# Kernel tuning notes

Hardware: AMD Instinct MI355X
Metric: run time of the kernel (lower is better)

Reference implementation:

```python
import jax, jax.numpy as jnp
import numpy as np
import math

B, S, D, H = 2, 2048, 2048, 16
HD = D // H  # head_dim = 128


def _rope_tables(seq_len, head_dim, theta=10000.0):
    inv = 1.0 / (theta ** (np.arange(0, head_dim, 2, dtype=np.float32) / head_dim))
    t = np.arange(seq_len, dtype=np.float32)
    freqs = np.outer(t, inv)  # [S, HD/2]
    return jnp.asarray(np.cos(freqs)), jnp.asarray(np.sin(freqs))


def setup_inputs() -> dict:
    key = jax.random.key(0)
    ks = jax.random.split(key, 6)
    std = 1.0 / math.sqrt(D)
    x = jax.random.normal(ks[0], (B, S, D), dtype=jnp.float32)
    wq_w = jax.random.normal(ks[1], (D, D), dtype=jnp.float32) * std
    wk_w = jax.random.normal(ks[2], (D, D), dtype=jnp.float32) * std
    wv_w = jax.random.normal(ks[3], (D, D), dtype=jnp.float32) * std
    wo_w = jax.random.normal(ks[4], (D, D), dtype=jnp.float32) * std
    zb = jnp.zeros((D,), dtype=jnp.float32)
    fc, fs = _rope_tables(S, HD)
    return {"x": x, "wq_w": wq_w, "wq_b": zb, "wk_w": wk_w, "wk_b": zb,
            "wv_w": wv_w, "wv_b": zb, "wo_w": wo_w, "wo_b": zb,
            "freqs_cos": fc, "freqs_sin": fs}


def _apply_rope(q, k, cos, sin):
    # q, k: [B, S, H, HD]; cos/sin: [S, HD/2] -> broadcast [1, S, 1, HD/2]
    cos = cos[None, :, None, :]
    sin = sin[None, :, None, :]

    def rot(t):
        tr, ti = t[..., 0::2], t[..., 1::2]
        orr = tr * cos - ti * sin
        oi = tr * sin + ti * cos
        return jnp.stack([orr, oi], axis=-1).reshape(t.shape)

    return rot(q), rot(k)


def reference(x, wq_w, wq_b, wk_w, wk_b, wv_w, wv_b, wo_w, wo_b, freqs_cos, freqs_sin):
    b, s, d = x.shape
    q = (x @ wq_w.T + wq_b).reshape(b, s, H, HD)
    k = (x @ wk_w.T + wk_b).reshape(b, s, H, HD)
    v = (x @ wv_w.T + wv_b).reshape(b, s, H, HD)
    q, k = _apply_rope(q, k, freqs_cos[:s], freqs_sin[:s])
    q = q.transpose(0, 2, 1, 3)  # [B,H,S,HD]
    k = k.transpose(0, 2, 1, 3)
    v = v.transpose(0, 2, 1, 3)
    scale = math.sqrt(HD)
    scores = jnp.einsum('bhqd,bhkd->bhqk', q, k) / scale
    causal = jnp.tril(jnp.ones((s, s), dtype=bool))
    scores = jnp.where(causal[None, None], scores, jnp.float32(-jnp.inf))
    attn = jax.nn.softmax(scores, axis=-1)
    out = jnp.einsum('bhqk,bhkd->bhqd', attn, v)
    out = out.transpose(0, 2, 1, 3).reshape(b, s, d)
    out = out @ wo_w.T + wo_b
    return out, k, v
```

## Files before the change

kernel.cpp:

```cpp
#include <hip/hip_runtime.h>

#define B_  2
#define S_  2048
#define D_  2048
#define H_  16
#define HD_ 128

#define QSCALE 0.1275174319003887f

typedef __attribute__((ext_vector_type(4))) float  f32x4;
typedef __attribute__((ext_vector_type(8))) short  short8;
typedef __attribute__((ext_vector_type(8))) __bf16 bf16x8;
typedef __attribute__((ext_vector_type(4))) float  floatv4;
typedef __attribute__((ext_vector_type(4))) unsigned short ushortv4;

__device__ inline unsigned short f2bf(float f) {
  unsigned int u = __builtin_bit_cast(unsigned int, f);
  u += 0x7fffu + ((u >> 16) & 1u);
  return (unsigned short)(u >> 16);
}

__device__ inline void gld16(void* lds, const void* g) {
  __builtin_amdgcn_global_load_lds(
      (const __attribute__((address_space(1))) unsigned int*)g,
      (__attribute__((address_space(3))) unsigned int*)lds, 16, 0, 0);
}

__device__ inline bf16x8 lds_frag(const unsigned short* p) {
  return __builtin_bit_cast(bf16x8, *(const short8*)p);
}
__device__ inline bf16x8 lds_frag_b(const void* p) {
  return __builtin_bit_cast(bf16x8, *(const short8*)p);
}

__global__ void cvt_all(const float* __restrict__ x,
                        const float* __restrict__ w0, const float* __restrict__ w1,
                        const float* __restrict__ w2, const float* __restrict__ w3,
                        unsigned short* __restrict__ xb,
                        unsigned short* __restrict__ wb0, unsigned short* __restrict__ wb1,
                        unsigned short* __restrict__ wb2, unsigned short* __restrict__ wb3) {
  int i = blockIdx.x * 256 + threadIdx.x;
  const float* s; unsigned short* d; int off;
  if (i < 2097152) { s = x; d = xb; off = i; }
  else {
    int j = i - 2097152;
    int r = j >> 20; off = j & 1048575;
    s = (r == 0) ? w0 : (r == 1) ? w1 : (r == 2) ? w2 : w3;
    d = (r == 0) ? wb0 : (r == 1) ? wb1 : (r == 2) ? wb2 : wb3;
  }
  floatv4 v = ((const floatv4*)s)[off];
  ushortv4 o;
  o.x = f2bf(v.x); o.y = f2bf(v.y); o.z = f2bf(v.z); o.w = f2bf(v.w);
  ((ushortv4*)d)[off] = o;
}

__global__ __launch_bounds__(256, 2)
void gemm_nt(const unsigned short* __restrict__ A,
             const unsigned short* __restrict__ W,
             const float* __restrict__ bias,
             float* __restrict__ C, int M, int N, int K) {
  __shared__ __attribute__((aligned(16))) unsigned short As[128 * 32];
  __shared__ __attribute__((aligned(16))) unsigned short Bs[128 * 32];
  const int t = threadIdx.x;
  const int w = t >> 6, lane = t & 63;
  const int quad = lane >> 4, l16 = lane & 15;
  const int m0 = blockIdx.y * 128, n0 = blockIdx.x * 128;
  const int wm = (w >> 1) * 64, wn = (w & 1) * 64;
  f32x4 acc[4][4] = {};

  for (int k0 = 0; k0 < K; k0 += 32) {
    __syncthreads();
#pragma unroll
    for (int j = 0; j < 2; ++j) {
      int o = (t + 256 * j) * 16;
      int row = o >> 6, cb = o & 63;
      gld16((char*)As + w * 1024 + j * 4096,
            (const char*)(A + (size_t)(m0 + row) * K + k0) + cb);
      gld16((char*)Bs + w * 1024 + j * 4096,
            (const char*)(W + (size_t)(n0 + row) * K + k0) + cb);
    }
    __syncthreads();
    bf16x8 af[4], bfr[4];
#pragma unroll
    for (int i = 0; i < 4; ++i)
      af[i] = lds_frag(As + (wm + i * 16 + l16) * 32 + quad * 8);
#pragma unroll
    for (int j = 0; j < 4; ++j)
      bfr[j] = lds_frag(Bs + (wn + j * 16 + l16) * 32 + quad * 8);
#pragma unroll
    for (int i = 0; i < 4; ++i)
#pragma unroll
      for (int j = 0; j < 4; ++j)
        acc[i][j] = __builtin_amdgcn_mfma_f32_16x16x32_bf16(af[i], bfr[j], acc[i][j], 0, 0, 0);
  }

#pragma unroll
  for (int j = 0; j < 4; ++j) {
    int col = n0 + wn + j * 16 + l16;
    float bv = bias[col];
#pragma unroll
    for (int i = 0; i < 4; ++i)
#pragma unroll
      for (int r = 0; r < 4; ++r) {
        int row = m0 + wm + i * 16 + quad * 4 + r;
        C[(size_t)row * N + col] = acc[i][j][r] + bv;
      }
  }
}

template<int MI0, int NJ0>
__device__ inline void quad_mm(f32x4 (&acc)[4][4], const bf16x8 (&af)[2][2], const bf16x8 (&bf)[2][2]) {
#pragma unroll
  for (int mi = 0; mi < 2; ++mi)
#pragma unroll
    for (int nj = 0; nj < 2; ++nj)
#pragma unroll
      for (int ks = 0; ks < 2; ++ks)
        acc[MI0 + mi][NJ0 + nj] =
            __builtin_amdgcn_mfma_f32_16x16x32_bf16(af[mi][ks], bf[nj][ks], acc[MI0 + mi][NJ0 + nj], 0, 0, 0);
}

__device__ inline void stage(char* ldsbuf, int chunk, const char* gtile, int w, long thrOff) {
  gld16(ldsbuf + chunk * 8192 + w * 1024, gtile + (long)chunk * 64 * 4096 + thrOff);
}

#define RDF(dst, buf, baserow)                                                          \
  do {                                                                                  \
    int _r0 = (baserow);                                                                \
    _Pragma("unroll") for (int _ii = 0; _ii < 2; ++_ii) {                               \
      int _row = _r0 + _ii * 16;                                                        \
      _Pragma("unroll") for (int _ks = 0; _ks < 2; ++_ks)                               \
          dst[_ii][_ks] = lds_frag_b((buf) + _row * 128 + ((_ks * 64 + quad * 16) ^ xsw)); \
    }                                                                                   \
  } while (0)

#define GBAR() __builtin_amdgcn_s_barrier()
#define LGK0()                                                 \
  do {                                                         \
    asm volatile("s_waitcnt lgkmcnt(0)" ::: "memory");         \
    __builtin_amdgcn_sched_barrier(0);                         \
  } while (0)

template<bool QKV>
__global__ __launch_bounds__(512, 1)
void gemm8p(const unsigned short* __restrict__ A,
            const unsigned short* __restrict__ W,
            const float* __restrict__ b0, const float* __restrict__ b1, const float* __restrict__ b2,
            float* __restrict__ C0, float* __restrict__ C1, float* __restrict__ C2,
            int nbx) {
  __shared__ __attribute__((aligned(16))) char smem[98304];
  char* As0 = smem;
  char* As1 = smem + 32768;
  char* Bs0 = smem + 65536;
  char* Bs1 = smem + 81920;

  const int t = threadIdx.x, w = t >> 6, lane = t & 63;
  const int quad = lane >> 4, l16 = lane & 15;
  const int wm = (w >> 1) * 64, wn = (w & 1) * 64;
  const int xsw = (l16 & 7) << 4;

  const int nwg = gridDim.x, q8 = nwg >> 3;
  const int wg = ((int)blockIdx.x & 7) * q8 + ((int)blockIdx.x >> 3);
  const int by = wg / nbx, bx = wg % nbx;
  const int m0 = by * 256, n0 = bx * 128;

  const char* Agl = (const char*)A + (size_t)m0 * 4096;
  const char* Wgl = (const char*)W + (size_t)n0 * 4096;
  const int sr = t >> 3;
  const long thrOff = (long)sr * 4096 + (((t & 7) * 16) ^ ((sr & 7) << 4));

#pragma unroll
  for (int c = 0; c < 4; ++c) stage(As0, c, Agl, w, thrOff);
#pragma unroll
  for (int c = 0; c < 2; ++c) stage(Bs0, c, Wgl, w, thrOff);
#pragma unroll
  for (int c = 0; c < 4; ++c) stage(As1, c, Agl + 128, w, thrOff);
#pragma unroll
  for (int c = 0; c < 2; ++c) stage(Bs1, c, Wgl + 128, w, thrOff);
  asm volatile("s_waitcnt vmcnt(6)" ::: "memory");
  GBAR();

  f32x4 acc[4][4] = {};

  for (int it = 0; it < 16; ++it) {
    int s0 = 2 * it + 2; if (s0 >= 32) s0 -= 2;
    int s1 = 2 * it + 3; if (s1 >= 32) s1 -= 2;
    const char* As0g = Agl + (long)s0 * 128;
    const char* Bs0g = Wgl + (long)s0 * 128;
    const char* As1g = Agl + (long)s1 * 128;
    const char* Bs1g = Wgl + (long)s1 * 128;
    bf16x8 a01[2][2], a23[2][2], b01[2][2], b23[2][2];

    RDF(a01, As0, wm + l16);
    RDF(b01, Bs0, wn + l16);
    GBAR(); LGK0();
    __builtin_amdgcn_s_setprio(1); quad_mm<0, 0>(acc, a01, b01); __builtin_amdgcn_s_setprio(0);
    GBAR();
    RDF(a23, As0, wm + 32 + l16);
    GBAR(); LGK0();
    __builtin_amdgcn_s_setprio(1); quad_mm<2, 0>(acc, a23, b01); __builtin_amdgcn_s_setprio(0);
    GBAR();
    RDF(b23, Bs0, wn + 32 + l16);
    stage(As0, 0, As0g, w, thrOff); stage(As0, 1, As0g, w, thrOff);
    GBAR(); LGK0();
    __builtin_amdgcn_s_setprio(1); quad_mm<0, 2>(acc, a01, b23); __builtin_amdgcn_s_setprio(0);
    GBAR();
    stage(As0, 2, As0g, w, thrOff); stage(As0, 3, As0g, w, thrOff);
    GBAR(); LGK0();
    __builtin_amdgcn_s_setprio(1); quad_mm<2, 2>(acc, a23, b23); __builtin_amdgcn_s_setprio(0);
    asm volatile("s_waitcnt vmcnt(4)" ::: "memory");
    GBAR();
    RDF(a01, As1, wm + l16);
    RDF(b01, Bs1, wn + l16);
    stage(Bs0, 0, Bs0g, w, thrOff); stage(Bs0, 1, Bs0g, w, thrOff);
    GBAR(); LGK0();
    __builtin_amdgcn_s_setprio(1); quad_mm<0, 0>(acc, a01, b01); __builtin_amdgcn_s_setprio(0);
    GBAR();
    RDF(a23, As1, wm + 32 + l16);
    GBAR(); LGK0();
    __builtin_amdgcn_s_setprio(1); quad_mm<2, 0>(acc, a23, b01); __builtin_amdgcn_s_setprio(0);
    GBAR();
    RDF(b23, Bs1, wn + 32 + l16);
    stage(As1, 0, As1g, w, thrOff); stage(As1, 1, As1g, w, thrOff);
    GBAR(); LGK0();
    __builtin_amdgcn_s_setprio(1); quad_mm<0, 2>(acc, a01, b23); __builtin_amdgcn_s_setprio(0);
    GBAR();
    stage(As1, 2, As1g, w, thrOff); stage(As1, 3, As1g, w, thrOff);
    stage(Bs1, 0, Bs1g, w, thrOff); stage(Bs1, 1, Bs1g, w, thrOff);
    GBAR(); LGK0();
    __builtin_amdgcn_s_setprio(1); quad_mm<2, 2>(acc, a23, b23); __builtin_amdgcn_s_setprio(0);
    asm volatile("s_waitcnt vmcnt(6)" ::: "memory");
    GBAR();
  }

  asm volatile("s_waitcnt vmcnt(0)" ::: "memory");

#pragma unroll
  for (int nj = 0; nj < 4; ++nj) {
    int col = n0 + wn + nj * 16 + l16;
    const float* bp; float* Cd; int cc;
    if constexpr (QKV) {
      int sel = col >> 11;
      bp = (sel == 0) ? b0 : (sel == 1) ? b1 : b2;
      Cd = (sel == 0) ? C0 : (sel == 1) ? C1 : C2;
      cc = col & 2047;
    } else {
      bp = b0; Cd = C0; cc = col;
    }
    float bv = bp[cc];
#pragma unroll
    for (int mi = 0; mi < 4; ++mi)
#pragma unroll
      for (int r = 0; r < 4; ++r) {
        int row = m0 + wm + mi * 16 + quad * 4 + r;
        Cd[(size_t)row * 2048 + cc] = acc[mi][nj][r] + bv;
      }
  }
}

__global__ void rope_kernel(const float* __restrict__ Qbuf,
                            const float* __restrict__ Kbuf,
                            const float* __restrict__ fc,
                            const float* __restrict__ fs,
                            unsigned short* __restrict__ Qa,
                            unsigned short* __restrict__ Ka,
                            float* __restrict__ k_out) {
  int idx = blockIdx.x * 256 + threadIdx.x;
  int i = idx & 63;
  int h = (idx >> 6) & (H_ - 1);
  int s = (idx >> 10) & (S_ - 1);
  int b = idx >> 21;
  size_t src = ((size_t)(b * S_ + s)) * D_ + h * HD_ + 2 * i;
  float2 q = *(const float2*)(Qbuf + src);
  float2 k = *(const float2*)(Kbuf + src);
  float c = fc[s * 64 + i], sn = fs[s * 64 + i];
  float qor = q.x * c - q.y * sn, qoi = q.x * sn + q.y * c;
  float kor = k.x * c - k.y * sn, koi = k.x * sn + k.y * c;
  size_t dst = ((size_t)((b * H_ + h) * S_ + s)) * HD_ + 2 * i;
  *(unsigned int*)(Qa + dst) = (unsigned int)f2bf(qor * QSCALE) | ((unsigned int)f2bf(qoi * QSCALE) << 16);
  *(unsigned int*)(Ka + dst) = (unsigned int)f2bf(kor) | ((unsigned int)f2bf(koi) << 16);
  *(float2*)(k_out + dst) = make_float2(kor, koi);
}

__global__ void vtrans_kernel(const float* __restrict__ Vbuf,
                              float* __restrict__ v_out,
                              unsigned short* __restrict__ Vt) {
  __shared__ float tile[64][33];
  int t = threadIdx.x;
  int s0 = blockIdx.x * 64, d0 = blockIdx.y * 32, bh = blockIdx.z;
  int b = bh >> 4, h = bh & 15;
#pragma unroll
  for (int rr = 0; rr < 8; ++rr) {
    int sl = rr * 8 + (t >> 5), dl = t & 31;
    float v = Vbuf[((size_t)(b * S_ + s0 + sl)) * D_ + h * HD_ + d0 + dl];
    tile[sl][dl] = v;
    v_out[((size_t)(bh * S_ + s0 + sl)) * HD_ + d0 + dl] = v;
  }
  __syncthreads();
#pragma unroll
  for (int rr = 0; rr < 8; ++rr) {
    int dl = rr * 4 + (t >> 6), sl = t & 63;
    Vt[((size_t)(bh * HD_ + d0 + dl)) * S_ + s0 + sl] = f2bf(tile[sl][dl]);
  }
}

__global__ __launch_bounds__(256, 2)
void attn_kernel(const unsigned short* __restrict__ Qa,
                 const unsigned short* __restrict__ Ka,
                 const unsigned short* __restrict__ Vt,
                 unsigned short* __restrict__ Oa) {
  __shared__ __attribute__((aligned(16))) unsigned short Ks[2][64 * 128];
  __shared__ __attribute__((aligned(16))) unsigned short Vs[128 * 64];
  __shared__ __attribute__((aligned(16))) unsigned short Ps[4][16 * 64];
  const int t = threadIdx.x, w = t >> 6, lane = t & 63;
  const int quad = lane >> 4, l16 = lane & 15;
  const int bid = blockIdx.x;
  const int bh = (bid & 7) + 8 * (bid >> 7);
  const int p  = (bid >> 3) & 15;
  const int b = bh >> 4, h = bh & 15;
  const unsigned short* Qp = Qa + (size_t)bh * S_ * HD_;
  const unsigned short* Kp = Ka + (size_t)bh * S_ * HD_;
  const unsigned short* Vp = Vt + (size_t)bh * HD_ * S_;
  const float NEGINF = -__builtin_inff();

  for (int part = 0; part < 2; ++part) {
    const int qs = part ? (31 - p) : p;
    const int q0 = qs * 64;
    const int ntmax = qs;

    __syncthreads();

#pragma unroll
    for (int j = 0; j < 4; ++j) {
      int o = (t + 256 * j) * 16;
      int row = o >> 8, cb = (o & 255) ^ ((row & 7) << 4);
      gld16((char*)Ks[0] + w * 1024 + j * 4096, (const char*)(Kp + (size_t)row * HD_) + cb);
    }
    bf16x8 qf[4];
#pragma unroll
    for (int kk = 0; kk < 4; ++kk)
      qf[kk] = *(const bf16x8*)(Qp + (size_t)(q0 + w * 16 + l16) * HD_ + kk * 32 + quad * 8);

    float m_i[4], l_i[4];
#pragma unroll
    for (int r = 0; r < 4; ++r) { m_i[r] = NEGINF; l_i[r] = 0.f; }
    f32x4 oacc[8] = {};
    int c = 0;

    for (int nt = 0; nt <= ntmax; ++nt) {
      __syncthreads();

#pragma unroll
      for (int j = 0; j < 4; ++j) {
        int o = (t + 256 * j) * 16;
        int vrow = o >> 7, vcb = (o & 127) ^ ((vrow & 7) << 4);
        gld16((char*)Vs + w * 1024 + j * 4096,
              (const char*)(Vp + (size_t)vrow * S_ + nt * 64) + vcb);
      }

      f32x4 sacc[4] = {};
      const char* Kc = (const char*)Ks[c];
#pragma unroll
      for (int j = 0; j < 4; ++j) {
        int krow = j * 16 + l16;
        const char* kbase = Kc + krow * 256;
        int ksw = (krow & 7) << 4;
#pragma unroll
        for (int kk = 0; kk < 4; ++kk) {
          bf16x8 kf = lds_frag_b(kbase + ((kk * 64 + quad * 16) ^ ksw));
          sacc[j] = __builtin_amdgcn_mfma_f32_16x16x32_bf16(qf[kk], kf, sacc[j], 0, 0, 0);
        }
      }

      const bool dotail = (nt == ntmax);
      float rowmax[4], alpha[4], rowsum[4];
#pragma unroll
      for (int r = 0; r < 4; ++r) rowmax[r] = NEGINF;
#pragma unroll
      for (int j = 0; j < 4; ++j) {
        int scol = nt * 64 + j * 16 + l16;
#pragma unroll
        for (int r = 0; r < 4; ++r) {
          float v = sacc[j][r];
          if (dotail && scol > q0 + w * 16 + quad * 4 + r) v = NEGINF;
          sacc[j][r] = v;
          rowmax[r] = fmaxf(rowmax[r], v);
        }
      }
#pragma unroll
      for (int off = 1; off < 16; off <<= 1)
#pragma unroll
        for (int r = 0; r < 4; ++r)
          rowmax[r] = fmaxf(rowmax[r], __shfl_xor(rowmax[r], off));
#pragma unroll
      for (int r = 0; r < 4; ++r) {
        float mnew = fmaxf(m_i[r], rowmax[r]);
        alpha[r] = __builtin_amdgcn_exp2f(m_i[r] - mnew);
        m_i[r] = mnew;
        rowsum[r] = 0.f;
      }
#pragma unroll
      for (int j = 0; j < 4; ++j)
#pragma unroll
        for (int r = 0; r < 4; ++r) {
          float e = __builtin_amdgcn_exp2f(sacc[j][r] - m_i[r]);
          sacc[j][r] = e;
          rowsum[r] += e;
        }
#pragma unroll
      for (int off = 1; off < 16; off <<= 1)
#pragma unroll
        for (int r = 0; r < 4; ++r)
          rowsum[r] += __shfl_xor(rowsum[r], off);
#pragma unroll
      for (int r = 0; r < 4; ++r) l_i[r] = l_i[r] * alpha[r] + rowsum[r];
#pragma unroll
      for (int f = 0; f < 8; ++f)
#pragma unroll
        for (int r = 0; r < 4; ++r) oacc[f][r] *= alpha[r];

      __syncthreads();

      if (nt < ntmax) {
#pragma unroll
        for (int j = 0; j < 4; ++j) {
          int o = (t + 256 * j) * 16;
          int row = o >> 8, cb = (o & 255) ^ ((row & 7) << 4);
          gld16((char*)Ks[c ^ 1] + w * 1024 + j * 4096,
                (const char*)(Kp + (size_t)((nt + 1) * 64 + row) * HD_) + cb);
        }
      }

      char* Pw = (char*)&Ps[w][0];
#pragma unroll
      for (int j = 0; j < 4; ++j)
#pragma unroll
        for (int r = 0; r < 4; ++r) {
          int prow = quad * 4 + r;
          *(unsigned short*)(Pw + prow * 128 + ((2 * (j * 16 + l16)) ^ ((prow & 7) << 4))) = f2bf(sacc[j][r]);
        }
      asm volatile("s_waitcnt lgkmcnt(0)" ::: "memory");

      const char* Vb = (const char*)Vs;
      int psw = (l16 & 7) << 4;
#pragma unroll
      for (int s2 = 0; s2 < 2; ++s2) {
        bf16x8 pf = lds_frag_b(Pw + l16 * 128 + ((s2 * 64 + quad * 16) ^ psw));
#pragma unroll
        for (int f = 0; f < 8; ++f) {
          int vrow = f * 16 + l16;
          bf16x8 vf = lds_frag_b(Vb + vrow * 128 + ((s2 * 64 + quad * 16) ^ ((vrow & 7) << 4)));
          oacc[f] = __builtin_amdgcn_mfma_f32_16x16x32_bf16(pf, vf, oacc[f], 0, 0, 0);
        }
      }
      c ^= 1;
    }

    float invl[4];
#pragma unroll
    for (int r = 0; r < 4; ++r) invl[r] = 1.f / l_i[r];
#pragma unroll
    for (int f = 0; f < 8; ++f)
#pragma unroll
      for (int r = 0; r < 4; ++r) {
        int srow = q0 + w * 16 + quad * 4 + r;
        int d = f * 16 + l16;
        Oa[((size_t)(b * S_ + srow)) * D_ + h * HD_ + d] = f2bf(oacc[f][r] * invl[r]);
      }
  }
}

extern "C" void kernel_launch(void* const* d_in, const int* in_sizes, int n_in,
                              void* d_out, int out_size, void* d_ws, size_t ws_size,
                              hipStream_t stream) {
  const float* x    = (const float*)d_in[0];
  const float* wq_w = (const float*)d_in[1];
  const float* wq_b = (const float*)d_in[2];
  const float* wk_w = (const float*)d_in[3];
  const float* wk_b = (const float*)d_in[4];
  const float* wv_w = (const float*)d_in[5];
  const float* wv_b = (const float*)d_in[6];
  const float* wo_w = (const float*)d_in[7];
  const float* wo_b = (const float*)d_in[8];
  const float* fc   = (const float*)d_in[9];
  const float* fs   = (const float*)d_in[10];

  float* out = (float*)d_out;
  const size_t BSD = (size_t)B_ * S_ * D_;
  float* k_out = out + BSD;
  float* v_out = out + 2 * BSD;

  char* ws = (char*)d_ws;
  unsigned short* xb   = (unsigned short*)(ws);
  unsigned short* wqb  = (unsigned short*)(ws + 16777216);
  unsigned short* wkb  = (unsigned short*)(ws + 25165824);
  unsigned short* wvb  = (unsigned short*)(ws + 33554432);
  unsigned short* wob  = (unsigned short*)(ws + 41943040);
  float*          Vbuf = (float*)(ws + 50331648);
  unsigned short* Qat  = (unsigned short*)(ws + 83886080);
  unsigned short* Kat  = (unsigned short*)(ws + 100663296);
  unsigned short* Vt   = (unsigned short*)(ws + 117440512);
  unsigned short* Ab   = (unsigned short*)(ws + 134217728);

  float* Qbuf = out;
  float* Kbuf = v_out;

  cvt_all<<<24576, 256, 0, stream>>>(x, wq_w, wk_w, wv_w, wo_w, xb, wqb, wkb, wvb, wob);

  gemm8p<true><<<dim3(768), 512, 0, stream>>>(xb, wqb, wq_b, wk_b, wv_b,
                                              Qbuf, Kbuf, Vbuf, 48);

  rope_kernel<<<16384, 256, 0, stream>>>(Qbuf, Kbuf, fc, fs, Qat, Kat, k_out);
  vtrans_kernel<<<dim3(32, 4, 32), 256, 0, stream>>>(Vbuf, v_out, Vt);
  attn_kernel<<<512, 256, 0, stream>>>(Qat, Kat, Vt, Ab);

  gemm_nt<<<dim3(16, 32), 256, 0, stream>>>(Ab, wob, wo_b, out, 4096, 2048, 2048);
}
```

Baseline: 451.6 us.

## Fuse RoPE and head-major scatter into QKV GEMM epilogue, reuse pipelined GEMM for output

The QKV GEMM epilogue now applies RoPE via a lane shuffle and writes bf16 Q/K and fp32 K/V directly in head-major layout. This removes the separate rope kernel and the fp32 Q/K/V round trip through global memory. The GEMM main loop is also rescheduled: the staging order changes and the MFMA quads are merged between fewer barriers. The simple output-projection GEMM is replaced by the 8-wave pipelined GEMM. The fused epilogue does scattered, non-coalesced stores per element and reloads the cos/sin tables, and the restructured pipeline carries risk around its wait counts.

```diff
diff --git a/kernel.cpp b/kernel.cpp
--- a/kernel.cpp
+++ b/kernel.cpp
@@ -26,9 +26,6 @@
       (__attribute__((address_space(3))) unsigned int*)lds, 16, 0, 0);
 }
 
-__device__ inline bf16x8 lds_frag(const unsigned short* p) {
-  return __builtin_bit_cast(bf16x8, *(const short8*)p);
-}
 __device__ inline bf16x8 lds_frag_b(const void* p) {
   return __builtin_bit_cast(bf16x8, *(const short8*)p);
 }
@@ -54,60 +51,6 @@
   ((ushortv4*)d)[off] = o;
 }
 
-__global__ __launch_bounds__(256, 2)
-void gemm_nt(const unsigned short* __restrict__ A,
-             const unsigned short* __restrict__ W,
-             const float* __restrict__ bias,
-             float* __restrict__ C, int M, int N, int K) {
-  __shared__ __attribute__((aligned(16))) unsigned short As[128 * 32];
-  __shared__ __attribute__((aligned(16))) unsigned short Bs[128 * 32];
-  const int t = threadIdx.x;
-  const int w = t >> 6, lane = t & 63;
-  const int quad = lane >> 4, l16 = lane & 15;
-  const int m0 = blockIdx.y * 128, n0 = blockIdx.x * 128;
-  const int wm = (w >> 1) * 64, wn = (w & 1) * 64;
-  f32x4 acc[4][4] = {};
-
-  for (int k0 = 0; k0 < K; k0 += 32) {
-    __syncthreads();
-#pragma unroll
-    for (int j = 0; j < 2; ++j) {
-      int o = (t + 256 * j) * 16;
-      int row = o >> 6, cb = o & 63;
-      gld16((char*)As + w * 1024 + j * 4096,
-            (const char*)(A + (size_t)(m0 + row) * K + k0) + cb);
-      gld16((char*)Bs + w * 1024 + j * 4096,
-            (const char*)(W + (size_t)(n0 + row) * K + k0) + cb);
-    }
-    __syncthreads();
-    bf16x8 af[4], bfr[4];
-#pragma unroll
-    for (int i = 0; i < 4; ++i)
-      af[i] = lds_frag(As + (wm + i * 16 + l16) * 32 + quad * 8);
-#pragma unroll
-    for (int j = 0; j < 4; ++j)
-      bfr[j] = lds_frag(Bs + (wn + j * 16 + l16) * 32 + quad * 8);
-#pragma unroll
-    for (int i = 0; i < 4; ++i)
-#pragma unroll
-      for (int j = 0; j < 4; ++j)
-        acc[i][j] = __builtin_amdgcn_mfma_f32_16x16x32_bf16(af[i], bfr[j], acc[i][j], 0, 0, 0);
-  }
-
-#pragma unroll
-  for (int j = 0; j < 4; ++j) {
-    int col = n0 + wn + j * 16 + l16;
-    float bv = bias[col];
-#pragma unroll
-    for (int i = 0; i < 4; ++i)
-#pragma unroll
-      for (int r = 0; r < 4; ++r) {
-        int row = m0 + wm + i * 16 + quad * 4 + r;
-        C[(size_t)row * N + col] = acc[i][j][r] + bv;
-      }
-  }
-}
-
 template<int MI0, int NJ0>
 __device__ inline void quad_mm(f32x4 (&acc)[4][4], const bf16x8 (&af)[2][2], const bf16x8 (&bf)[2][2]) {
 #pragma unroll
@@ -141,12 +84,15 @@
     __builtin_amdgcn_sched_barrier(0);                         \
   } while (0)
 
-template<bool QKV>
+template<int MODE>
 __global__ __launch_bounds__(512, 1)
 void gemm8p(const unsigned short* __restrict__ A,
             const unsigned short* __restrict__ W,
             const float* __restrict__ b0, const float* __restrict__ b1, const float* __restrict__ b2,
-            float* __restrict__ C0, float* __restrict__ C1, float* __restrict__ C2,
+            float* __restrict__ C0,
+            unsigned short* __restrict__ Qat, unsigned short* __restrict__ Kat,
+            float* __restrict__ k_out, float* __restrict__ v_out,
+            const float* __restrict__ fc, const float* __restrict__ fs,
             int nbx) {
   __shared__ __attribute__((aligned(16))) char smem[98304];
   char* As0 = smem;
@@ -175,126 +121,118 @@
   for (int c = 0; c < 2; ++c) stage(Bs0, c, Wgl, w, thrOff);
 #pragma unroll
   for (int c = 0; c < 4; ++c) stage(As1, c, Agl + 128, w, thrOff);
-#pragma unroll
-  for (int c = 0; c < 2; ++c) stage(Bs1, c, Wgl + 128, w, thrOff);
-  asm volatile("s_waitcnt vmcnt(6)" ::: "memory");
+  asm volatile("s_waitcnt vmcnt(4)" ::: "memory");
   GBAR();
 
   f32x4 acc[4][4] = {};
 
   for (int it = 0; it < 16; ++it) {
-    int s0 = 2 * it + 2; if (s0 >= 32) s0 -= 2;
-    int s1 = 2 * it + 3; if (s1 >= 32) s1 -= 2;
-    const char* As0g = Agl + (long)s0 * 128;
-    const char* Bs0g = Wgl + (long)s0 * 128;
-    const char* As1g = Agl + (long)s1 * 128;
-    const char* Bs1g = Wgl + (long)s1 * 128;
+    int s0p = 2 * it + 2; if (s0p >= 32) s0p -= 2;
+    int s1p = 2 * it + 3; if (s1p >= 32) s1p -= 2;
+    const char* gB1  = Wgl + (long)(2 * it + 1) * 128;
+    const char* gA0p = Agl + (long)s0p * 128;
+    const char* gB0p = Wgl + (long)s0p * 128;
+    const char* gA1p = Agl + (long)s1p * 128;
     bf16x8 a01[2][2], a23[2][2], b01[2][2], b23[2][2];
 
+    stage(Bs1, 0, gB1, w, thrOff); stage(Bs1, 1, gB1, w, thrOff);
     RDF(a01, As0, wm + l16);
+    RDF(a23, As0, wm + 32 + l16);
     RDF(b01, Bs0, wn + l16);
     GBAR(); LGK0();
-    __builtin_amdgcn_s_setprio(1); quad_mm<0, 0>(acc, a01, b01); __builtin_amdgcn_s_setprio(0);
-    GBAR();
-    RDF(a23, As0, wm + 32 + l16);
-    GBAR(); LGK0();
-    __builtin_amdgcn_s_setprio(1); quad_mm<2, 0>(acc, a23, b01); __builtin_amdgcn_s_setprio(0);
+    __builtin_amdgcn_s_setprio(1);
+    quad_mm<0, 0>(acc, a01, b01); quad_mm<2, 0>(acc, a23, b01);
+    __builtin_amdgcn_s_setprio(0);
     GBAR();
     RDF(b23, Bs0, wn + 32 + l16);
-    stage(As0, 0, As0g, w, thrOff); stage(As0, 1, As0g, w, thrOff);
+    stage(As0, 0, gA0p, w, thrOff); stage(As0, 1, gA0p, w, thrOff);
+    stage(As0, 2, gA0p, w, thrOff); stage(As0, 3, gA0p, w, thrOff);
     GBAR(); LGK0();
-    __builtin_amdgcn_s_setprio(1); quad_mm<0, 2>(acc, a01, b23); __builtin_amdgcn_s_setprio(0);
-    GBAR();
-    stage(As0, 2, As0g, w, thrOff); stage(As0, 3, As0g, w, thrOff);
-    GBAR(); LGK0();
-    __builtin_amdgcn_s_setprio(1); quad_mm<2, 2>(acc, a23, b23); __builtin_amdgcn_s_setprio(0);
+    __builtin_amdgcn_s_setprio(1);
+    quad_mm<0, 2>(acc, a01, b23); quad_mm<2, 2>(acc, a23, b23);
+    __builtin_amdgcn_s_setprio(0);
     asm volatile("s_waitcnt vmcnt(4)" ::: "memory");
     GBAR();
     RDF(a01, As1, wm + l16);
+    RDF(a23, As1, wm + 32 + l16);
     RDF(b01, Bs1, wn + l16);
-    stage(Bs0, 0, Bs0g, w, thrOff); stage(Bs0, 1, Bs0g, w, thrOff);
+    stage(Bs0, 0, gB0p, w, thrOff); stage(Bs0, 1, gB0p, w, thrOff);
     GBAR(); LGK0();
-    __builtin_amdgcn_s_setprio(1); quad_mm<0, 0>(acc, a01, b01); __builtin_amdgcn_s_setprio(0);
-    GBAR();
-    RDF(a23, As1, wm + 32 + l16);
-    GBAR(); LGK0();
-    __builtin_amdgcn_s_setprio(1); quad_mm<2, 0>(acc, a23, b01); __builtin_amdgcn_s_setprio(0);
+    __builtin_amdgcn_s_setprio(1);
+    quad_mm<0, 0>(acc, a01, b01); quad_mm<2, 0>(acc, a23, b01);
+    __builtin_amdgcn_s_setprio(0);
     GBAR();
     RDF(b23, Bs1, wn + 32 + l16);
-    stage(As1, 0, As1g, w, thrOff); stage(As1, 1, As1g, w, thrOff);
+    stage(As1, 0, gA1p, w, thrOff); stage(As1, 1, gA1p, w, thrOff);
+    stage(As1, 2, gA1p, w, thrOff); stage(As1, 3, gA1p, w, thrOff);
     GBAR(); LGK0();
-    __builtin_amdgcn_s_setprio(1); quad_mm<0, 2>(acc, a01, b23); __builtin_amdgcn_s_setprio(0);
+    __builtin_amdgcn_s_setprio(1);
+    quad_mm<0, 2>(acc, a01, b23); quad_mm<2, 2>(acc, a23, b23);
+    __builtin_amdgcn_s_setprio(0);
+    asm volatile("s_waitcnt vmcnt(4)" ::: "memory");
     GBAR();
-    stage(As1, 2, As1g, w, thrOff); stage(As1, 3, As1g, w, thrOff);
-    stage(Bs1, 0, Bs1g, w, thrOff); stage(Bs1, 1, Bs1g, w, thrOff);
-    GBAR(); LGK0();
-    __builtin_amdgcn_s_setprio(1); quad_mm<2, 2>(acc, a23, b23); __builtin_amdgcn_s_setprio(0);
-    asm volatile("s_waitcnt vmcnt(6)" ::: "memory");
-    GBAR();
   }
 
   asm volatile("s_waitcnt vmcnt(0)" ::: "memory");
 
-#pragma unroll
-  for (int nj = 0; nj < 4; ++nj) {
-    int col = n0 + wn + nj * 16 + l16;
-    const float* bp; float* Cd; int cc;
-    if constexpr (QKV) {
+  if constexpr (MODE == 1) {
+#pragma unroll
+    for (int nj = 0; nj < 4; ++nj) {
+      int col = n0 + wn + nj * 16 + l16;
       int sel = col >> 11;
-      bp = (sel == 0) ? b0 : (sel == 1) ? b1 : b2;
-      Cd = (sel == 0) ? C0 : (sel == 1) ? C1 : C2;
-      cc = col & 2047;
-    } else {
-      bp = b0; Cd = C0; cc = col;
+      int cc  = col & 2047;
+      const float* bp = (sel == 0) ? b0 : (sel == 1) ? b1 : b2;
+      float bv = bp[cc];
+      int hh = cc >> 7, d = cc & 127, ii = d >> 1;
+      float ssel = (d & 1) ? 1.f : -1.f;
+#pragma unroll
+      for (int mi = 0; mi < 4; ++mi)
+#pragma unroll
+        for (int r = 0; r < 4; ++r) {
+          int row = m0 + wm + mi * 16 + quad * 4 + r;
+          int s = row & 2047, bb = row >> 11;
+          size_t dst = ((size_t)(bb * H_ + hh) * S_ + s) * HD_ + d;
+          float v = acc[mi][nj][r] + bv;
+          if (sel == 2) {
+            v_out[dst] = v;
+          } else {
+            float pv = __shfl_xor(v, 1);
+            float cs = fc[s * 64 + ii], sn = fs[s * 64 + ii];
+            float o = v * cs + pv * sn * ssel;
+            if (sel == 0) {
+              Qat[dst] = f2bf(o * QSCALE);
+            } else {
+              Kat[dst] = f2bf(o);
+              k_out[dst] = o;
+            }
+          }
+        }
     }
-    float bv = bp[cc];
-#pragma unroll
-    for (int mi = 0; mi < 4; ++mi)
-#pragma unroll
-      for (int r = 0; r < 4; ++r) {
-        int row = m0 + wm + mi * 16 + quad * 4 + r;
-        Cd[(size_t)row * 2048 + cc] = acc[mi][nj][r] + bv;
-      }
-  }
-}
-
-__global__ void rope_kernel(const float* __restrict__ Qbuf,
-                            const float* __restrict__ Kbuf,
-                            const float* __restrict__ fc,
-                            const float* __restrict__ fs,
-                            unsigned short* __restrict__ Qa,
-                            unsigned short* __restrict__ Ka,
-                            float* __restrict__ k_out) {
-  int idx = blockIdx.x * 256 + threadIdx.x;
-  int i = idx & 63;
-  int h = (idx >> 6) & (H_ - 1);
-  int s = (idx >> 10) & (S_ - 1);
-  int b = idx >> 21;
-  size_t src = ((size_t)(b * S_ + s)) * D_ + h * HD_ + 2 * i;
-  float2 q = *(const float2*)(Qbuf + src);
-  float2 k = *(const float2*)(Kbuf + src);
-  float c = fc[s * 64 + i], sn = fs[s * 64 + i];
-  float qor = q.x * c - q.y * sn, qoi = q.x * sn + q.y * c;
-  float kor = k.x * c - k.y * sn, koi = k.x * sn + k.y * c;
-  size_t dst = ((size_t)((b * H_ + h) * S_ + s)) * HD_ + 2 * i;
-  *(unsigned int*)(Qa + dst) = (unsigned int)f2bf(qor * QSCALE) | ((unsigned int)f2bf(qoi * QSCALE) << 16);
-  *(unsigned int*)(Ka + dst) = (unsigned int)f2bf(kor) | ((unsigned int)f2bf(koi) << 16);
-  *(float2*)(k_out + dst) = make_float2(kor, koi);
-}
-
-__global__ void vtrans_kernel(const float* __restrict__ Vbuf,
-                              float* __restrict__ v_out,
+  } else {
+#pragma unroll
+    for (int nj = 0; nj < 4; ++nj) {
+      int col = n0 + wn + nj * 16 + l16;
+      float bv = b0[col];
+#pragma unroll
+      for (int mi = 0; mi < 4; ++mi)
+#pragma unroll
+        for (int r = 0; r < 4; ++r) {
+          int row = m0 + wm + mi * 16 + quad * 4 + r;
+          C0[(size_t)row * 2048 + col] = acc[mi][nj][r] + bv;
+        }
+    }
+  }
+}
+
+__global__ void vtrans_kernel(const float* __restrict__ Vsrc,
                               unsigned short* __restrict__ Vt) {
   __shared__ float tile[64][33];
   int t = threadIdx.x;
   int s0 = blockIdx.x * 64, d0 = blockIdx.y * 32, bh = blockIdx.z;
-  int b = bh >> 4, h = bh & 15;
 #pragma unroll
   for (int rr = 0; rr < 8; ++rr) {
     int sl = rr * 8 + (t >> 5), dl = t & 31;
-    float v = Vbuf[((size_t)(b * S_ + s0 + sl)) * D_ + h * HD_ + d0 + dl];
-    tile[sl][dl] = v;
-    v_out[((size_t)(bh * S_ + s0 + sl)) * HD_ + d0 + dl] = v;
+    tile[sl][dl] = Vsrc[((size_t)(bh * S_ + s0 + sl)) * HD_ + d0 + dl];
   }
   __syncthreads();
 #pragma unroll
@@ -496,23 +434,20 @@
   unsigned short* wkb  = (unsigned short*)(ws + 25165824);
   unsigned short* wvb  = (unsigned short*)(ws + 33554432);
   unsigned short* wob  = (unsigned short*)(ws + 41943040);
-  float*          Vbuf = (float*)(ws + 50331648);
   unsigned short* Qat  = (unsigned short*)(ws + 83886080);
   unsigned short* Kat  = (unsigned short*)(ws + 100663296);
   unsigned short* Vt   = (unsigned short*)(ws + 117440512);
   unsigned short* Ab   = (unsigned short*)(ws + 134217728);
 
-  float* Qbuf = out;
-  float* Kbuf = v_out;
-
   cvt_all<<<24576, 256, 0, stream>>>(x, wq_w, wk_w, wv_w, wo_w, xb, wqb, wkb, wvb, wob);
 
-  gemm8p<true><<<dim3(768), 512, 0, stream>>>(xb, wqb, wq_b, wk_b, wv_b,
-                                              Qbuf, Kbuf, Vbuf, 48);
-
-  rope_kernel<<<16384, 256, 0, stream>>>(Qbuf, Kbuf, fc, fs, Qat, Kat, k_out);
-  vtrans_kernel<<<dim3(32, 4, 32), 256, 0, stream>>>(Vbuf, v_out, Vt);
+  gemm8p<1><<<dim3(768), 512, 0, stream>>>(xb, wqb, wq_b, wk_b, wv_b,
+                                           nullptr, Qat, Kat, k_out, v_out, fc, fs, 48);
+
+  vtrans_kernel<<<dim3(32, 4, 32), 256, 0, stream>>>(v_out, Vt);
   attn_kernel<<<512, 256, 0, stream>>>(Qat, Kat, Vt, Ab);
 
-  gemm_nt<<<dim3(16, 32), 256, 0, stream>>>(Ab, wob, wo_b, out, 4096, 2048, 2048);
-}
+  gemm8p<0><<<dim3(256), 512, 0, stream>>>(Ab, wob, wo_b, nullptr, nullptr,
+                                           out, nullptr, nullptr, nullptr, nullptr,
+                                           nullptr, nullptr, 16);
+}
```

Result: no change. 459.8 us (+1.8%).
